# Kernel tuning notes

Hardware: AMD Instinct MI355X
Metric: run time of the kernel (lower is better)

The kernel has to match this reference:

```python
import jax, jax.numpy as jnp
import numpy as np

N_NODES = 50000
N_EDGES = 800000
HIDDEN = 64
NUM_FEATURES = 1
OUT_DIM = 2


def setup_inputs() -> dict:
    key = jax.random.key(0)
    k = jax.random.split(key, 6)
    x = jax.random.normal(k[0], (N_NODES, NUM_FEATURES), dtype=jnp.float32)
    edge_index = jax.random.randint(k[1], (2, N_EDGES), 0, N_NODES, dtype=jnp.int32)
    # GCNConv params (PyG default: glorot weight, zero bias; random here for testing)
    W1 = jax.random.normal(k[2], (NUM_FEATURES, HIDDEN), dtype=jnp.float32) * 0.5
    b1 = jax.random.normal(k[3], (HIDDEN,), dtype=jnp.float32) * 0.1
    W2 = jax.random.normal(k[4], (HIDDEN, OUT_DIM), dtype=jnp.float32) * 0.1
    b2 = jax.random.normal(k[5], (OUT_DIM,), dtype=jnp.float32) * 0.1
    return {"x": x, "edge_index": edge_index, "W1": W1, "b1": b1, "W2": W2, "b2": b2}


def _gcn_norm(edge_index, num_nodes):
    # PyG gcn_norm with add_self_loops=True, symmetric normalization
    row, col = edge_index[0], edge_index[1]
    loop = jnp.arange(num_nodes, dtype=row.dtype)
    row = jnp.concatenate([row, loop])
    col = jnp.concatenate([col, loop])
    ew = jnp.ones(row.shape[0], dtype=jnp.float32)
    deg = jax.ops.segment_sum(ew, col, num_segments=num_nodes)  # in-degree incl. self-loop
    dinv = jnp.where(deg > 0, jax.lax.rsqrt(deg), 0.0)
    norm = dinv[row] * dinv[col]  # [E+N]
    return row, col, norm


def _gcn_conv(x, row, col, norm, W, b, num_nodes):
    h = x @ W                                  # [N, out] transform first (out <= in here is fine)
    msg = h[row] * norm[:, None]               # gather + scale, [E+N, out]
    out = jax.ops.segment_sum(msg, col, num_segments=num_nodes)  # scatter-add at targets
    return out + b


def reference(x, edge_index, W1, b1, W2, b2):
    row, col, norm = _gcn_norm(edge_index, N_NODES)
    h = _gcn_conv(x, row, col, norm, W1, b1, N_NODES)
    h = jax.nn.relu(h)
    out = _gcn_conv(h, row, col, norm, W2, b2, N_NODES)
    return out
```

## Files before the change

kernel.cpp:

```cpp
#include <hip/hip_runtime.h>
#include <math.h>

#define N_NODES 50000
#define N_EDGES 800000
#define HIDDEN  64
#define MAXDEG  64


__global__ __launch_bounds__(256)
void k_build(const int* __restrict__ row, const int* __restrict__ col,
             int* __restrict__ cnt, unsigned short* __restrict__ ell) {
    int i = blockIdx.x * blockDim.x + threadIdx.x;
    int e = i * 2;
    if (e + 1 < N_EDGES) {
        int2 c2 = *(const int2*)(col + e);
        int2 r2 = *(const int2*)(row + e);
        int rk0 = atomicAdd(&cnt[c2.x], 1);
        int rk1 = atomicAdd(&cnt[c2.y], 1);
        if (rk0 < MAXDEG) ell[rk0 * N_NODES + c2.x] = (unsigned short)r2.x;
        if (rk1 < MAXDEG) ell[rk1 * N_NODES + c2.y] = (unsigned short)r2.y;
    } else if (e < N_EDGES) {
        int c = col[e];
        int rk = atomicAdd(&cnt[c], 1);
        if (rk < MAXDEG) ell[rk * N_NODES + c] = (unsigned short)row[e];
    }
}

__global__ __launch_bounds__(256)
void k_layer1(const unsigned short* __restrict__ ell, const int* __restrict__ cnt,
              const float* __restrict__ x,
              const float* __restrict__ W1, const float* __restrict__ b1,
              const float* __restrict__ W2, float2* __restrict__ z) {
    int n = blockIdx.x * blockDim.x + threadIdx.x;
    if (n >= N_NODES) return;
    int d = cnt[n]; if (d > MAXDEG) d = MAXDEG;
    float acc = 0.0f;
    int j = 0;
    for (; j + 2 <= d; j += 2) {
        int r0 = ell[j * N_NODES + n];
        int r1 = ell[(j + 1) * N_NODES + n];
        float g0 = rsqrtf((float)(cnt[r0] + 1)) * x[r0];
        float g1 = rsqrtf((float)(cnt[r1] + 1)) * x[r1];
        acc += g0 + g1;
    }
    if (j < d) {
        int r = ell[j * N_NODES + n];
        acc += rsqrtf((float)(cnt[r] + 1)) * x[r];
    }
    float di = rsqrtf((float)(d + 1));
    float sv = di * (acc + di * x[n]);
    float y0 = 0.0f, y1 = 0.0f;
#pragma unroll
    for (int k = 0; k < HIDDEN; ++k) {
        float h = fmaxf(sv * W1[k] + b1[k], 0.0f);
        y0 += h * W2[2 * k];
        y1 += h * W2[2 * k + 1];
    }
    z[n] = make_float2(di * y0, di * y1);
}

__global__ __launch_bounds__(256)
void k_layer2(const unsigned short* __restrict__ ell, const int* __restrict__ cnt,
              const float2* __restrict__ z, const float* __restrict__ b2,
              float2* __restrict__ out) {
    int n = blockIdx.x * blockDim.x + threadIdx.x;
    if (n >= N_NODES) return;
    int d = cnt[n]; if (d > MAXDEG) d = MAXDEG;
    float T0 = 0.0f, T1 = 0.0f;
    int j = 0;
    for (; j + 2 <= d; j += 2) {
        int r0 = ell[j * N_NODES + n];
        int r1 = ell[(j + 1) * N_NODES + n];
        float2 v0 = z[r0], v1 = z[r1];
        T0 += v0.x + v1.x;
        T1 += v0.y + v1.y;
    }
    if (j < d) {
        float2 v = z[ell[j * N_NODES + n]];
        T0 += v.x; T1 += v.y;
    }
    float di = rsqrtf((float)(d + 1));
    float2 zn = z[n];
    out[n] = make_float2(di * (T0 + zn.x) + b2[0], di * (T1 + zn.y) + b2[1]);
}


extern "C" void kernel_launch(void* const* d_in, const int* in_sizes, int n_in,
                              void* d_out, int out_size, void* d_ws, size_t ws_size,
                              hipStream_t stream) {
    const float* x  = (const float*)d_in[0];
    const int*   ei = (const int*)d_in[1];
    const float* W1 = (const float*)d_in[2];
    const float* b1 = (const float*)d_in[3];
    const float* W2 = (const float*)d_in[4];
    const float* b2 = (const float*)d_in[5];

    const int* row = ei;
    const int* col = ei + N_EDGES;

    int*    ws  = (int*)d_ws;
    int*    cnt = ws;
    float2* z   = (float2*)(ws + N_NODES);
    unsigned short* ell = (unsigned short*)(ws + 3 * N_NODES);

    const int gE = (N_EDGES / 2 + 255) / 256;
    const int gN = (N_NODES + 255) / 256;

    hipMemsetAsync(cnt, 0, N_NODES * sizeof(int), stream);
    k_build <<<gE, 256, 0, stream>>>(row, col, cnt, ell);
    k_layer1<<<gN, 256, 0, stream>>>(ell, cnt, x, W1, b1, W2, z);
    k_layer2<<<gN, 256, 0, stream>>>(ell, cnt, z, b2, (float2*)d_out);
}
```

Baseline: 128.3 us.

## Split neighbor aggregation across four wavefronts per node and precompute scaled features

```diff
diff --git a/kernel.cpp b/kernel.cpp
--- a/kernel.cpp
+++ b/kernel.cpp
@@ -5,6 +5,7 @@
 #define N_EDGES 800000
 #define HIDDEN  64
 #define MAXDEG  64
+#define NPB     64
 
 
 __global__ __launch_bounds__(256)
@@ -27,61 +28,68 @@
 }
 
 __global__ __launch_bounds__(256)
+void k_g(const int* __restrict__ cnt, const float* __restrict__ x,
+         float* __restrict__ g) {
+    int i = blockIdx.x * blockDim.x + threadIdx.x;
+    if (i < N_NODES) g[i] = rsqrtf((float)(min(cnt[i], MAXDEG) + 1)) * x[i];
+}
+
+__global__ __launch_bounds__(256)
 void k_layer1(const unsigned short* __restrict__ ell, const int* __restrict__ cnt,
-              const float* __restrict__ x,
+              const float* __restrict__ g,
               const float* __restrict__ W1, const float* __restrict__ b1,
               const float* __restrict__ W2, float2* __restrict__ z) {
-    int n = blockIdx.x * blockDim.x + threadIdx.x;
-    if (n >= N_NODES) return;
-    int d = cnt[n]; if (d > MAXDEG) d = MAXDEG;
+    __shared__ float red[4][NPB];
+    const int w = threadIdx.x >> 6;
+    const int l = threadIdx.x & 63;
+    const int n = blockIdx.x * NPB + l;
+    const bool valid = (n < N_NODES);
+    int d = valid ? min(cnt[n], MAXDEG) : 0;
     float acc = 0.0f;
-    int j = 0;
-    for (; j + 2 <= d; j += 2) {
-        int r0 = ell[j * N_NODES + n];
-        int r1 = ell[(j + 1) * N_NODES + n];
-        float g0 = rsqrtf((float)(cnt[r0] + 1)) * x[r0];
-        float g1 = rsqrtf((float)(cnt[r1] + 1)) * x[r1];
-        acc += g0 + g1;
+    for (int j = w; j < d; j += 4)
+        acc += g[ell[j * N_NODES + n]];
+    red[w][l] = acc;
+    __syncthreads();
+    if (w == 0 && valid) {
+        float a  = red[0][l] + red[1][l] + red[2][l] + red[3][l];
+        float di = rsqrtf((float)(d + 1));
+        float sv = di * (a + g[n]);
+        float y0 = 0.0f, y1 = 0.0f;
+#pragma unroll
+        for (int k = 0; k < HIDDEN; ++k) {
+            float h = fmaxf(sv * W1[k] + b1[k], 0.0f);
+            y0 += h * W2[2 * k];
+            y1 += h * W2[2 * k + 1];
+        }
+        z[n] = make_float2(di * y0, di * y1);
     }
-    if (j < d) {
-        int r = ell[j * N_NODES + n];
-        acc += rsqrtf((float)(cnt[r] + 1)) * x[r];
-    }
-    float di = rsqrtf((float)(d + 1));
-    float sv = di * (acc + di * x[n]);
-    float y0 = 0.0f, y1 = 0.0f;
-#pragma unroll
-    for (int k = 0; k < HIDDEN; ++k) {
-        float h = fmaxf(sv * W1[k] + b1[k], 0.0f);
-        y0 += h * W2[2 * k];
-        y1 += h * W2[2 * k + 1];
-    }
-    z[n] = make_float2(di * y0, di * y1);
 }
 
 __global__ __launch_bounds__(256)
 void k_layer2(const unsigned short* __restrict__ ell, const int* __restrict__ cnt,
               const float2* __restrict__ z, const float* __restrict__ b2,
               float2* __restrict__ out) {
-    int n = blockIdx.x * blockDim.x + threadIdx.x;
-    if (n >= N_NODES) return;
-    int d = cnt[n]; if (d > MAXDEG) d = MAXDEG;
+    __shared__ float2 red[4][NPB];
+    const int w = threadIdx.x >> 6;
+    const int l = threadIdx.x & 63;
+    const int n = blockIdx.x * NPB + l;
+    const bool valid = (n < N_NODES);
+    int d = valid ? min(cnt[n], MAXDEG) : 0;
     float T0 = 0.0f, T1 = 0.0f;
-    int j = 0;
-    for (; j + 2 <= d; j += 2) {
-        int r0 = ell[j * N_NODES + n];
-        int r1 = ell[(j + 1) * N_NODES + n];
-        float2 v0 = z[r0], v1 = z[r1];
-        T0 += v0.x + v1.x;
-        T1 += v0.y + v1.y;
-    }
-    if (j < d) {
+    for (int j = w; j < d; j += 4) {
         float2 v = z[ell[j * N_NODES + n]];
         T0 += v.x; T1 += v.y;
     }
-    float di = rsqrtf((float)(d + 1));
-    float2 zn = z[n];
-    out[n] = make_float2(di * (T0 + zn.x) + b2[0], di * (T1 + zn.y) + b2[1]);
+    red[w][l] = make_float2(T0, T1);
+    __syncthreads();
+    if (w == 0 && valid) {
+        float2 a0 = red[0][l], a1 = red[1][l], a2 = red[2][l], a3 = red[3][l];
+        float Tx = a0.x + a1.x + a2.x + a3.x;
+        float Ty = a0.y + a1.y + a2.y + a3.y;
+        float di = rsqrtf((float)(d + 1));
+        float2 zn = z[n];
+        out[n] = make_float2(di * (Tx + zn.x) + b2[0], di * (Ty + zn.y) + b2[1]);
+    }
 }
 
 
@@ -100,14 +108,17 @@
 
     int*    ws  = (int*)d_ws;
     int*    cnt = ws;
-    float2* z   = (float2*)(ws + N_NODES);
-    unsigned short* ell = (unsigned short*)(ws + 3 * N_NODES);
+    float*  g   = (float*)(ws + N_NODES);
+    float2* z   = (float2*)(ws + 2 * N_NODES);
+    unsigned short* ell = (unsigned short*)(ws + 4 * N_NODES);
 
     const int gE = (N_EDGES / 2 + 255) / 256;
     const int gN = (N_NODES + 255) / 256;
+    const int gL = (N_NODES + NPB - 1) / NPB;
 
     hipMemsetAsync(cnt, 0, N_NODES * sizeof(int), stream);
     k_build <<<gE, 256, 0, stream>>>(row, col, cnt, ell);
-    k_layer1<<<gN, 256, 0, stream>>>(ell, cnt, x, W1, b1, W2, z);
-    k_layer2<<<gN, 256, 0, stream>>>(ell, cnt, z, b2, (float2*)d_out);
+    k_g     <<<gN, 256, 0, stream>>>(cnt, x, g);
+    k_layer1<<<gL, 256, 0, stream>>>(ell, cnt, g, W1, b1, W2, z);
+    k_layer2<<<gL, 256, 0, stream>>>(ell, cnt, z, b2, (float2*)d_out);
 }
```

After: 124.1 us. 3.3% less time.
